# Kernel optimization log

Hardware: AMD Instinct MI355X
Metric: run time of the kernel (lower is better)

Reference implementation:

```python
import jax, jax.numpy as jnp
import numpy as np

V, B, T, D, F, E = 16000, 8, 1024, 64, 256, 8


def setup_inputs() -> dict:
    key = jax.random.key(0)
    ks = jax.random.split(key, 8)
    s = 0.02
    return {
        "x": jax.random.randint(ks[0], (B, T), 0, V),
        "embed_table": jax.random.normal(ks[1], (V, D), jnp.float32) * s,
        "Wm": jax.random.normal(ks[2], (D, D), jnp.float32) * s,
        "Um": jax.random.normal(ks[3], (D, D), jnp.float32) * s,
        "bm": jnp.zeros((D,), jnp.float32),
        "Wg": jax.random.normal(ks[4], (D, E), jnp.float32) * s,
        "bg": jnp.zeros((E,), jnp.float32),
        "W1": jax.random.normal(ks[5], (E, D, F), jnp.float32) * s,
        "b1": jnp.zeros((E, F), jnp.float32),
        "W2": jax.random.normal(ks[6], (E, F, D), jnp.float32) * s,
        "b2": jnp.zeros((E, D), jnp.float32),
        "ln_g": jnp.ones((D,), jnp.float32),
        "ln_b": jnp.zeros((D,), jnp.float32),
        "head_W": jax.random.normal(ks[7], (D, V), jnp.float32) * s,
        "head_b": jnp.zeros((V,), jnp.float32),
    }


def _layernorm(y, g, b, eps=1e-5):
    mu = jnp.mean(y, axis=-1, keepdims=True)
    var = jnp.mean((y - mu) ** 2, axis=-1, keepdims=True)
    return g * (y - mu) * jax.lax.rsqrt(var + eps) + b


def reference(x, embed_table, Wm, Um, bm, Wg, bg, W1, b1, W2, b2, ln_g, ln_b, head_W, head_b):
    emb = embed_table[x]                    # [B, T, D]
    emb_t = jnp.swapaxes(emb, 0, 1)         # [T, B, D] for scan over time

    def step(mem, x_t):
        # recurrent router: state update then gate computation
        mem_new = jnp.tanh(x_t @ Wm + mem @ Um + bm)              # [B, D]
        gates = jax.nn.softmax(mem_new @ Wg + bg, axis=-1)        # [B, E]
        # all-experts dense FFN (exact erf GELU as in torch default)
        h = jax.nn.gelu(jnp.einsum('bd,edf->bef', x_t, W1) + b1, approximate=False)
        eo = jnp.einsum('bef,efd->bed', h, W2) + b2               # [B, E, D]
        moe = jnp.einsum('be,bed->bd', gates, eo)                 # gated sum
        out_t = _layernorm(x_t + moe, ln_g, ln_b)
        return mem_new, out_t

    mem0 = jnp.zeros((x.shape[0], emb.shape[-1]), emb.dtype)
    _, outs = jax.lax.scan(step, mem0, emb_t)   # outs: [T, B, D]
    out = jnp.swapaxes(outs, 0, 1)              # [B, T, D]
    logits = out @ head_W + head_b              # [B, T, V]
    # training_mode=False -> no pred_loss branch; avg_pred_loss == 0.0
    return logits
```

## Files before the change

kernel.cpp:

```cpp
#include <hip/hip_runtime.h>


#define VV 16000
#define BB 8
#define TT 1024
#define DD 64
#define FF 256
#define EE 8
#define BT 8192

typedef unsigned short u16;
typedef unsigned int   u32;
typedef __attribute__((ext_vector_type(8))) short short8;
typedef __attribute__((ext_vector_type(4))) float f32x4;
typedef __attribute__((ext_vector_type(2))) float f32x2;

__device__ __forceinline__ float bf2f(u16 u) {
    union { u32 i; float f; } v; v.i = ((u32)u) << 16; return v.f;
}
__device__ __forceinline__ u16 f2bf(float f) {
    union { float f; u32 i; } v; v.f = f;
    u32 lsb = (v.i >> 16) & 1u;
    return (u16)((v.i + 0x7fffu + lsb) >> 16);
}
__device__ __forceinline__ short8 ld8(const u16* p) { return *(const short8*)p; }
__device__ __forceinline__ float ldf(const void* p, int i, int isbf) {
    return isbf ? bf2f(((const u16*)p)[i]) : ((const float*)p)[i];
}

__global__ __launch_bounds__(256) void k_sniff(const u32* __restrict__ tblw,
                                               int* __restrict__ flag) {
    __shared__ int c;
    int tid = threadIdx.x;
    if (tid == 0) c = 0;
    __syncthreads();
    u32 u = tblw[tid];
    u32 lo = u & 0xFFFFu;
    u32 e = (lo >> 7) & 0xFFu;
    int hit = ((e >= 0x60u && e <= 0x7Eu) || lo == 0u) ? 1 : 0;
    atomicAdd(&c, hit);
    __syncthreads();
    if (tid == 0) *flag = (c >= 192) ? 1 : 0;
}

__global__ __launch_bounds__(256) void k_transph(const void* __restrict__ headW,
                                                 const int* __restrict__ flag,
                                                 u16* __restrict__ headWT) {
    __shared__ float tile[DD][DD + 1];
    int isbf = *flag;
    int v0 = blockIdx.x * 64;
    int tid = threadIdx.x;
    int c = tid & 63, rq = tid >> 6;
#pragma unroll
    for (int i = 0; i < 16; i++) {
        int k = i * 4 + rq;
        tile[k][c] = ldf(headW, k * VV + v0 + c, isbf);
    }
    __syncthreads();
#pragma unroll
    for (int i = 0; i < 16; i++) {
        int v = i * 4 + rq;
        headWT[(v0 + v) * DD + c] = f2bf(tile[c][v]);
    }
}

__global__ __launch_bounds__(256) void k_transpose(const void* __restrict__ W1,
                                                   const void* __restrict__ W2,
                                                   const int* __restrict__ flag,
                                                   u16* __restrict__ W1T,
                                                   u16* __restrict__ W2T) {
    int isbf = *flag;
    int idx = blockIdx.x * 256 + threadIdx.x;
    if (idx < EE * DD * FF) {
        int e = idx >> 14, r = idx & 16383, d = r >> 8, f = r & 255;
        W1T[e * 16384 + f * DD + d] = f2bf(ldf(W1, idx, isbf));
    } else {
        int j2 = idx - EE * DD * FF;
        int e = j2 >> 14, r = j2 & 16383, f = r >> 6, d = r & 63;
        W2T[e * 16384 + d * FF + f] = f2bf(ldf(W2, j2, isbf));
    }
}

__global__ __launch_bounds__(256) void k_embed_pre(const int* __restrict__ x,
                                                   const void* __restrict__ tbl,
                                                   const void* __restrict__ Wm,
                                                   const void* __restrict__ bm,
                                                   const int* __restrict__ flag,
                                                   u16* __restrict__ emb,
                                                   float* __restrict__ pre) {
    __shared__ float sWm[DD * DD];
    __shared__ float sbm[DD];
    int isbf = *flag;
    int tid = threadIdx.x;
    for (int i = tid; i < DD * DD; i += 256) sWm[i] = ldf(Wm, i, isbf);
    if (tid < DD) sbm[tid] = ldf(bm, tid, isbf);
    __syncthreads();

    int gi = blockIdx.x * 256 + tid;
    int tok = gi >> 2, q = gi & 3;
    int id = x[tok];
    float e[DD];
    if (isbf) {
        const uint4* src = (const uint4*)((const u16*)tbl + id * DD);
        uint4* dst = (uint4*)(emb + tok * DD);
#pragma unroll
        for (int i = 0; i < 8; i++) {
            uint4 v = src[i];
            if ((i >> 1) == q) dst[i] = v;
            const u16* pu = (const u16*)&v;
#pragma unroll
            for (int j = 0; j < 8; j++) e[i * 8 + j] = bf2f(pu[j]);
        }
    } else {
        const float4* src = (const float4*)((const float*)tbl + id * DD);
        u16* dst = emb + tok * DD;
#pragma unroll
        for (int i = 0; i < 16; i++) {
            float4 v = src[i];
            e[i * 4 + 0] = v.x; e[i * 4 + 1] = v.y;
            e[i * 4 + 2] = v.z; e[i * 4 + 3] = v.w;
            if ((i >> 2) == q) {
                u32 p0 = (u32)f2bf(v.x) | ((u32)f2bf(v.y) << 16);
                u32 p1 = (u32)f2bf(v.z) | ((u32)f2bf(v.w) << 16);
                ((u32*)dst)[i * 2] = p0;
                ((u32*)dst)[i * 2 + 1] = p1;
            }
        }
    }
    int b = tok >> 10, t = tok & 1023;
    float* prow = pre + (t * BB + b) * DD + q * 16;
#pragma unroll
    for (int j4 = 0; j4 < 4; j4++) {
        int j0 = q * 16 + j4 * 4;
        float a0 = sbm[j0 + 0], a1 = sbm[j0 + 1];
        float a2 = sbm[j0 + 2], a3 = sbm[j0 + 3];
#pragma unroll
        for (int k = 0; k < DD; k++) {
            float ek = e[k];
            float4 wv = *(const float4*)&sWm[k * DD + j0];
            a0 += ek * wv.x; a1 += ek * wv.y;
            a2 += ek * wv.z; a3 += ek * wv.w;
        }
        ((float4*)prow)[j4] = make_float4(a0, a1, a2, a3);
    }
}

__global__ __launch_bounds__(256, 1) void k_scan_ffn(
        const float* __restrict__ pre, const void* __restrict__ Um,
        const u16* __restrict__ emb, const u16* __restrict__ W1T,
        const void* __restrict__ b1g, const u16* __restrict__ W2T,
        const void* __restrict__ b2g, const int* __restrict__ flag,
        float* __restrict__ mem, u16* __restrict__ eo) {
    __shared__ u16 hh[4][16 * 264];
    int isbf = *flag;
    int bid = blockIdx.x;

    if (bid < BB) {
        if (threadIdx.x >= 64) return;
        int b = bid, j = threadIdx.x;
        float* sm = (float*)hh;

        f32x2 c0, c1, c2, c3, c4, c5, c6, c7, c8, c9, c10, c11, c12, c13,
              c14, c15, c16, c17, c18, c19, c20, c21, c22, c23, c24, c25,
              c26, c27, c28, c29, c30, c31;
        if (isbf) {
            const u16* up = (const u16*)Um + j;
#define LDU(VAR, I) VAR = (f32x2){bf2f(up[(2 * I) * DD]), bf2f(up[(2 * I + 1) * DD])};
            LDU(c0, 0)  LDU(c1, 1)  LDU(c2, 2)  LDU(c3, 3)
            LDU(c4, 4)  LDU(c5, 5)  LDU(c6, 6)  LDU(c7, 7)
            LDU(c8, 8)  LDU(c9, 9)  LDU(c10, 10) LDU(c11, 11)
            LDU(c12, 12) LDU(c13, 13) LDU(c14, 14) LDU(c15, 15)
            LDU(c16, 16) LDU(c17, 17) LDU(c18, 18) LDU(c19, 19)
            LDU(c20, 20) LDU(c21, 21) LDU(c22, 22) LDU(c23, 23)
            LDU(c24, 24) LDU(c25, 25) LDU(c26, 26) LDU(c27, 27)
            LDU(c28, 28) LDU(c29, 29) LDU(c30, 30) LDU(c31, 31)
#undef LDU
        } else {
            const float* up = (const float*)Um + j;
#define LDU(VAR, I) VAR = (f32x2){up[(2 * I) * DD], up[(2 * I + 1) * DD]};
            LDU(c0, 0)  LDU(c1, 1)  LDU(c2, 2)  LDU(c3, 3)
            LDU(c4, 4)  LDU(c5, 5)  LDU(c6, 6)  LDU(c7, 7)
            LDU(c8, 8)  LDU(c9, 9)  LDU(c10, 10) LDU(c11, 11)
            LDU(c12, 12) LDU(c13, 13) LDU(c14, 14) LDU(c15, 15)
            LDU(c16, 16) LDU(c17, 17) LDU(c18, 18) LDU(c19, 19)
            LDU(c20, 20) LDU(c21, 21) LDU(c22, 22) LDU(c23, 23)
            LDU(c24, 24) LDU(c25, 25) LDU(c26, 26) LDU(c27, 27)
            LDU(c28, 28) LDU(c29, 29) LDU(c30, 30) LDU(c31, 31)
#undef LDU
        }
        asm volatile("" : "+v"(c0), "+v"(c1), "+v"(c2), "+v"(c3),
                          "+v"(c4), "+v"(c5), "+v"(c6), "+v"(c7));
        asm volatile("" : "+v"(c8), "+v"(c9), "+v"(c10), "+v"(c11),
                          "+v"(c12), "+v"(c13), "+v"(c14), "+v"(c15));
        asm volatile("" : "+v"(c16), "+v"(c17), "+v"(c18), "+v"(c19),
                          "+v"(c20), "+v"(c21), "+v"(c22), "+v"(c23));
        asm volatile("" : "+v"(c24), "+v"(c25), "+v"(c26), "+v"(c27),
                          "+v"(c28), "+v"(c29), "+v"(c30), "+v"(c31));
        sm[j] = 0.f;

        float pcur = pre[b * DD + j];
        for (int t = 0; t < TT; t++) {
            int tn = (t + 1 < TT) ? t + 1 : t;
            float pnext = pre[(tn * BB + b) * DD + j];
            const f32x4* mv = (const f32x4*)sm;
            f32x2 A0 = {0.f, 0.f}, A1 = {0.f, 0.f};
            f32x2 A2 = {0.f, 0.f}, A3 = {0.f, 0.f};
#define STEP2(KK, UA, UB, UC, UD) {                             \
            f32x4 va = mv[2 * KK], vb = mv[2 * KK + 1];         \
            A0 += __builtin_shufflevector(va, va, 0, 1) * UA;   \
            A1 += __builtin_shufflevector(va, va, 2, 3) * UB;   \
            A2 += __builtin_shufflevector(vb, vb, 0, 1) * UC;   \
            A3 += __builtin_shufflevector(vb, vb, 2, 3) * UD; }
            STEP2(0, c0, c1, c2, c3)     STEP2(1, c4, c5, c6, c7)
            STEP2(2, c8, c9, c10, c11)   STEP2(3, c12, c13, c14, c15)
            STEP2(4, c16, c17, c18, c19) STEP2(5, c20, c21, c22, c23)
            STEP2(6, c24, c25, c26, c27) STEP2(7, c28, c29, c30, c31)
#undef STEP2
            float s = ((A0.x + A0.y) + (A1.x + A1.y))
                    + ((A2.x + A2.y) + (A3.x + A3.y)) + pcur;
            float ex = __expf(2.f * s);
            float mn = 1.f - 2.f * __builtin_amdgcn_rcpf(ex + 1.f);
            sm[j] = mn;
            mem[(t * BB + b) * DD + j] = mn;
            pcur = pnext;
        }
        return;
    }

    int fid = bid - BB;
    int e = fid >> 7, mb = fid & 127;
    int w = threadIdx.x >> 6, l = threadIdx.x & 63;
    int lr = l & 15, lq = l >> 4;
    int m0 = mb * 64 + w * 16;

    short8 a0 = ld8(emb + (m0 + lr) * DD + lq * 8);
    short8 a1 = ld8(emb + (m0 + lr) * DD + 32 + lq * 8);
    const u16* w1 = W1T + e * 16384;

    f32x4 acc[16];
#pragma unroll
    for (int nt = 0; nt < 16; nt++) {
        int n = nt * 16 + lr;
        short8 bf0 = ld8(w1 + n * DD + lq * 8);
        short8 bf1 = ld8(w1 + n * DD + 32 + lq * 8);
        f32x4 c = {0.f, 0.f, 0.f, 0.f};
        c = __builtin_amdgcn_mfma_f32_16x16x32_bf16(a0, bf0, c, 0, 0, 0);
        c = __builtin_amdgcn_mfma_f32_16x16x32_bf16(a1, bf1, c, 0, 0, 0);
        acc[nt] = c;
    }
    u16* hw = hh[w];
#pragma unroll
    for (int nt = 0; nt < 16; nt++) {
        int n = nt * 16 + lr;
        float bb = ldf(b1g, e * FF + n, isbf);
#pragma unroll
        for (int r = 0; r < 4; r++) {
            float xv = acc[nt][r] + bb;
            float g = 0.5f * xv * (1.f + erff(xv * 0.70710678118654752f));
            hw[(lq * 4 + r) * 264 + n] = f2bf(g);
        }
    }
    __syncthreads();

    f32x4 acc2[4];
#pragma unroll
    for (int dt = 0; dt < 4; dt++) acc2[dt] = (f32x4){0.f, 0.f, 0.f, 0.f};
    const u16* w2 = W2T + e * 16384;
#pragma unroll
    for (int kb = 0; kb < 8; kb++) {
        short8 af = ld8(hw + lr * 264 + kb * 32 + lq * 8);
#pragma unroll
        for (int dt = 0; dt < 4; dt++) {
            short8 bf = ld8(w2 + (dt * 16 + lr) * FF + kb * 32 + lq * 8);
            acc2[dt] = __builtin_amdgcn_mfma_f32_16x16x32_bf16(af, bf, acc2[dt], 0, 0, 0);
        }
    }
#pragma unroll
    for (int dt = 0; dt < 4; dt++) {
        int d = dt * 16 + lr;
        float bb = ldf(b2g, e * DD + d, isbf);
#pragma unroll
        for (int r = 0; r < 4; r++) {
            int tok = m0 + lq * 4 + r;
            eo[(tok * EE + e) * DD + d] = f2bf(acc2[dt][r] + bb);
        }
    }
}

__global__ __launch_bounds__(256) void k_gates(const float* __restrict__ mem,
                                               const void* __restrict__ Wg,
                                               const void* __restrict__ bg,
                                               const int* __restrict__ flag,
                                               float* __restrict__ gates) {
    __shared__ float sWg[DD * EE];
    int isbf = *flag;
    int tid = threadIdx.x;
    for (int i = tid; i < DD * EE; i += 256) sWg[i] = ldf(Wg, i, isbf);
    __syncthreads();

    int tok = blockIdx.x * 256 + tid;
    int b = tok >> 10, t = tok & 1023;
    const float* mr = mem + (t * BB + b) * DD;
    float z[EE];
#pragma unroll
    for (int e = 0; e < EE; e++) z[e] = ldf(bg, e, isbf);
    const float4* wg4 = (const float4*)sWg;
    const float4* mr4 = (const float4*)mr;
    for (int k4 = 0; k4 < 16; k4++) {
        float4 mv = mr4[k4];
        float m[4] = {mv.x, mv.y, mv.z, mv.w};
#pragma unroll
        for (int kk = 0; kk < 4; kk++) {
            int k = k4 * 4 + kk;
            float4 wa = wg4[k * 2], wb = wg4[k * 2 + 1];
            z[0] += m[kk] * wa.x; z[1] += m[kk] * wa.y;
            z[2] += m[kk] * wa.z; z[3] += m[kk] * wa.w;
            z[4] += m[kk] * wb.x; z[5] += m[kk] * wb.y;
            z[6] += m[kk] * wb.z; z[7] += m[kk] * wb.w;
        }
    }
    float zm = z[0];
#pragma unroll
    for (int e = 1; e < EE; e++) zm = fmaxf(zm, z[e]);
    float sum = 0.f;
#pragma unroll
    for (int e = 0; e < EE; e++) { z[e] = __expf(z[e] - zm); sum += z[e]; }
    float rs = __builtin_amdgcn_rcpf(sum);
#pragma unroll
    for (int e = 0; e < EE; e++) gates[tok * EE + e] = z[e] * rs;
}

__global__ __launch_bounds__(256) void k_ln(const u16* __restrict__ emb,
                                            const u16* __restrict__ eo,
                                            const float* __restrict__ gates,
                                            const void* __restrict__ ln_g,
                                            const void* __restrict__ ln_b,
                                            const int* __restrict__ flag,
                                            u16* __restrict__ outb) {
    int isbf = *flag;
    int w = threadIdx.x >> 6, l = threadIdx.x & 63;
    int tok = blockIdx.x * 4 + w;
    const float* g = gates + tok * EE;
    const u16* er = eo + tok * EE * DD;
    float moe = 0.f;
#pragma unroll
    for (int e = 0; e < EE; e++) moe += g[e] * bf2f(er[e * DD + l]);
    float y = bf2f(emb[tok * DD + l]) + moe;
    float s = y;
#pragma unroll
    for (int off = 32; off > 0; off >>= 1) s += __shfl_xor(s, off, 64);
    float mu = s * (1.f / 64.f);
    float d = y - mu;
    float s2 = d * d;
#pragma unroll
    for (int off = 32; off > 0; off >>= 1) s2 += __shfl_xor(s2, off, 64);
    float var = s2 * (1.f / 64.f);
    float r = rsqrtf(var + 1e-5f);
    float o = ldf(ln_g, l, isbf) * d * r + ldf(ln_b, l, isbf);
    outb[tok * DD + l] = f2bf(o);
}

__global__ __launch_bounds__(256) void k_head(const u16* __restrict__ outb,
                                              const u16* __restrict__ headWT,
                                              const void* __restrict__ head_b,
                                              const int* __restrict__ flag,
                                              void* __restrict__ logits) {
    int isbf = *flag;
    int nb = blockIdx.x, mb = blockIdx.y;
    int w = threadIdx.x >> 6, l = threadIdx.x & 63;
    int lr = l & 15, lq = l >> 4;
    int m0 = mb * 64 + w * 16;
    int n0 = nb * 256;
    int ntc = (nb == 62) ? 8 : 16;

    short8 a0 = ld8(outb + (m0 + lr) * DD + lq * 8);
    short8 a1 = ld8(outb + (m0 + lr) * DD + 32 + lq * 8);

    for (int nt = 0; nt < ntc; nt++) {
        int n = n0 + nt * 16 + lr;
        short8 bf0 = ld8(headWT + n * DD + lq * 8);
        short8 bf1 = ld8(headWT + n * DD + 32 + lq * 8);
        f32x4 c = {0.f, 0.f, 0.f, 0.f};
        c = __builtin_amdgcn_mfma_f32_16x16x32_bf16(a0, bf0, c, 0, 0, 0);
        c = __builtin_amdgcn_mfma_f32_16x16x32_bf16(a1, bf1, c, 0, 0, 0);
        float hb = ldf(head_b, n, isbf);
        if (isbf) {
#pragma unroll
            for (int r = 0; r < 4; r++)
                ((u16*)logits)[(m0 + lq * 4 + r) * VV + n] = f2bf(c[r] + hb);
        } else {
#pragma unroll
            for (int r = 0; r < 4; r++)
                ((float*)logits)[(m0 + lq * 4 + r) * VV + n] = c[r] + hb;
        }
    }
}

extern "C" void kernel_launch(void* const* d_in, const int* in_sizes, int n_in,
                              void* d_out, int out_size, void* d_ws, size_t ws_size,
                              hipStream_t stream) {
    const int*  x      = (const int*)d_in[0];
    const void* tbl    = d_in[1];
    const void* Wm     = d_in[2];
    const void* Um     = d_in[3];
    const void* bm     = d_in[4];
    const void* Wg     = d_in[5];
    const void* bg     = d_in[6];
    const void* W1     = d_in[7];
    const void* b1     = d_in[8];
    const void* W2     = d_in[9];
    const void* b2     = d_in[10];
    const void* ln_g   = d_in[11];
    const void* ln_b   = d_in[12];
    const void* headW  = d_in[13];
    const void* head_b = d_in[14];

    char* w = (char*)d_ws;
    int*   flag   = (int*)(w);
    u16*   headWT = (u16*)(w + 0x0000100);
    u16*   W1T    = (u16*)(w + 0x0200000);
    u16*   W2T    = (u16*)(w + 0x0240000);
    u16*   emb    = (u16*)(w + 0x0280000);
    u16*   outb   = (u16*)(w + 0x0380000);
    float* pre    = (float*)(w + 0x0480000);
    float* mem    = (float*)(w + 0x0680000);
    float* gates  = (float*)(w + 0x0880000);
    u16*   eo     = (u16*)(w + 0x08C0000);

    k_sniff<<<dim3(1), dim3(256), 0, stream>>>((const u32*)tbl, flag);
    k_transph<<<dim3(VV / 64), dim3(256), 0, stream>>>(headW, flag, headWT);
    k_transpose<<<dim3(2 * EE * DD * FF / 256), dim3(256), 0, stream>>>(
        W1, W2, flag, W1T, W2T);
    k_embed_pre<<<dim3(BT * 4 / 256), dim3(256), 0, stream>>>(x, tbl, Wm, bm, flag, emb, pre);
    k_scan_ffn<<<dim3(BB + EE * (BT / 64)), dim3(256), 0, stream>>>(
        pre, Um, emb, W1T, b1, W2T, b2, flag, mem, eo);
    k_gates<<<dim3(BT / 256), dim3(256), 0, stream>>>(mem, Wg, bg, flag, gates);
    k_ln<<<dim3(BT / 4), dim3(256), 0, stream>>>(emb, eo, gates, ln_g, ln_b, flag, outb);
    k_head<<<dim3(63, BT / 64), dim3(256), 0, stream>>>(outb, headWT, head_b, flag, d_out);
}
```

Measured before the change: 975.0 us.

## Pipeline scan, FFN, gates, LN and head across time chunks in a mega-kernel

Merges the embed/pre-projection, head-weight transpose and expert-weight transpose into one launch. The recurrent scan is split into four 256-step chunks, and a single multi-role kernel is launched seven times in a software-pipelined schedule: while chunk c is being scanned, the FFN, gates, layernorm and head GEMM run on earlier chunks. The aim is to hide the serial scan latency behind the parallel FFN and head work, which previously waited for the whole scan to finish. The cost is extra launches and some redundant scan setup per chunk, plus chunk-dependent indexing.

```diff
diff --git a/kernel.cpp b/kernel.cpp
--- a/kernel.cpp
+++ b/kernel.cpp
@@ -8,6 +8,7 @@
 #define FF 256
 #define EE 8
 #define BT 8192
+#define CT 256
 
 typedef unsigned short u16;
 typedef unsigned int   u32;
@@ -43,34 +44,100 @@
     if (tid == 0) *flag = (c >= 192) ? 1 : 0;
 }
 
-__global__ __launch_bounds__(256) void k_transph(const void* __restrict__ headW,
-                                                 const int* __restrict__ flag,
-                                                 u16* __restrict__ headWT) {
-    __shared__ float tile[DD][DD + 1];
+__global__ __launch_bounds__(256) void k_pre(const int* __restrict__ x,
+                                             const void* __restrict__ tbl,
+                                             const void* __restrict__ Wm,
+                                             const void* __restrict__ bm,
+                                             const void* __restrict__ headW,
+                                             const void* __restrict__ W1,
+                                             const void* __restrict__ W2,
+                                             const int* __restrict__ flag,
+                                             u16* __restrict__ emb,
+                                             float* __restrict__ pre,
+                                             u16* __restrict__ headWT,
+                                             u16* __restrict__ W1T,
+                                             u16* __restrict__ W2T) {
+    __shared__ float smem[4160];
     int isbf = *flag;
-    int v0 = blockIdx.x * 64;
+    int bid = blockIdx.x;
     int tid = threadIdx.x;
-    int c = tid & 63, rq = tid >> 6;
-#pragma unroll
-    for (int i = 0; i < 16; i++) {
-        int k = i * 4 + rq;
-        tile[k][c] = ldf(headW, k * VV + v0 + c, isbf);
-    }
-    __syncthreads();
-#pragma unroll
-    for (int i = 0; i < 16; i++) {
-        int v = i * 4 + rq;
-        headWT[(v0 + v) * DD + c] = f2bf(tile[c][v]);
-    }
-}
-
-__global__ __launch_bounds__(256) void k_transpose(const void* __restrict__ W1,
-                                                   const void* __restrict__ W2,
-                                                   const int* __restrict__ flag,
-                                                   u16* __restrict__ W1T,
-                                                   u16* __restrict__ W2T) {
-    int isbf = *flag;
-    int idx = blockIdx.x * 256 + threadIdx.x;
+
+    if (bid < 128) {
+        float* sWm = smem;
+        float* sbm = smem + 4096;
+        for (int i = tid; i < DD * DD; i += 256) sWm[i] = ldf(Wm, i, isbf);
+        if (tid < DD) sbm[tid] = ldf(bm, tid, isbf);
+        __syncthreads();
+
+        int gi = bid * 256 + tid;
+        int tok = gi >> 2, q = gi & 3;
+        int id = x[tok];
+        float e[DD];
+        if (isbf) {
+            const uint4* src = (const uint4*)((const u16*)tbl + id * DD);
+            uint4* dst = (uint4*)(emb + tok * DD);
+#pragma unroll
+            for (int i = 0; i < 8; i++) {
+                uint4 v = src[i];
+                if ((i >> 1) == q) dst[i] = v;
+                const u16* pu = (const u16*)&v;
+#pragma unroll
+                for (int j = 0; j < 8; j++) e[i * 8 + j] = bf2f(pu[j]);
+            }
+        } else {
+            const float4* src = (const float4*)((const float*)tbl + id * DD);
+            u16* dst = emb + tok * DD;
+#pragma unroll
+            for (int i = 0; i < 16; i++) {
+                float4 v = src[i];
+                e[i * 4 + 0] = v.x; e[i * 4 + 1] = v.y;
+                e[i * 4 + 2] = v.z; e[i * 4 + 3] = v.w;
+                if ((i >> 2) == q) {
+                    u32 p0 = (u32)f2bf(v.x) | ((u32)f2bf(v.y) << 16);
+                    u32 p1 = (u32)f2bf(v.z) | ((u32)f2bf(v.w) << 16);
+                    ((u32*)dst)[i * 2] = p0;
+                    ((u32*)dst)[i * 2 + 1] = p1;
+                }
+            }
+        }
+        int b = tok >> 10, t = tok & 1023;
+        float* prow = pre + (t * BB + b) * DD + q * 16;
+#pragma unroll
+        for (int j4 = 0; j4 < 4; j4++) {
+            int j0 = q * 16 + j4 * 4;
+            float a0 = sbm[j0 + 0], a1 = sbm[j0 + 1];
+            float a2 = sbm[j0 + 2], a3 = sbm[j0 + 3];
+#pragma unroll
+            for (int k = 0; k < DD; k++) {
+                float ek = e[k];
+                float4 wv = *(const float4*)&sWm[k * DD + j0];
+                a0 += ek * wv.x; a1 += ek * wv.y;
+                a2 += ek * wv.z; a3 += ek * wv.w;
+            }
+            ((float4*)prow)[j4] = make_float4(a0, a1, a2, a3);
+        }
+        return;
+    }
+
+    if (bid < 128 + 250) {
+        float (*tile)[DD + 1] = (float(*)[DD + 1])smem;
+        int v0 = (bid - 128) * 64;
+        int c = tid & 63, rq = tid >> 6;
+#pragma unroll
+        for (int i = 0; i < 16; i++) {
+            int k = i * 4 + rq;
+            tile[k][c] = ldf(headW, k * VV + v0 + c, isbf);
+        }
+        __syncthreads();
+#pragma unroll
+        for (int i = 0; i < 16; i++) {
+            int v = i * 4 + rq;
+            headWT[(v0 + v) * DD + c] = f2bf(tile[c][v]);
+        }
+        return;
+    }
+
+    int idx = (bid - 378) * 256 + tid;
     if (idx < EE * DD * FF) {
         int e = idx >> 14, r = idx & 16383, d = r >> 8, f = r & 255;
         W1T[e * 16384 + f * DD + d] = f2bf(ldf(W1, idx, isbf));
@@ -81,317 +148,266 @@
     }
 }
 
-__global__ __launch_bounds__(256) void k_embed_pre(const int* __restrict__ x,
-                                                   const void* __restrict__ tbl,
-                                                   const void* __restrict__ Wm,
-                                                   const void* __restrict__ bm,
-                                                   const int* __restrict__ flag,
-                                                   u16* __restrict__ emb,
-                                                   float* __restrict__ pre) {
-    __shared__ float sWm[DD * DD];
-    __shared__ float sbm[DD];
-    int isbf = *flag;
-    int tid = threadIdx.x;
-    for (int i = tid; i < DD * DD; i += 256) sWm[i] = ldf(Wm, i, isbf);
-    if (tid < DD) sbm[tid] = ldf(bm, tid, isbf);
-    __syncthreads();
-
-    int gi = blockIdx.x * 256 + tid;
-    int tok = gi >> 2, q = gi & 3;
-    int id = x[tok];
-    float e[DD];
-    if (isbf) {
-        const uint4* src = (const uint4*)((const u16*)tbl + id * DD);
-        uint4* dst = (uint4*)(emb + tok * DD);
-#pragma unroll
-        for (int i = 0; i < 8; i++) {
-            uint4 v = src[i];
-            if ((i >> 1) == q) dst[i] = v;
-            const u16* pu = (const u16*)&v;
-#pragma unroll
-            for (int j = 0; j < 8; j++) e[i * 8 + j] = bf2f(pu[j]);
-        }
-    } else {
-        const float4* src = (const float4*)((const float*)tbl + id * DD);
-        u16* dst = emb + tok * DD;
-#pragma unroll
-        for (int i = 0; i < 16; i++) {
-            float4 v = src[i];
-            e[i * 4 + 0] = v.x; e[i * 4 + 1] = v.y;
-            e[i * 4 + 2] = v.z; e[i * 4 + 3] = v.w;
-            if ((i >> 2) == q) {
-                u32 p0 = (u32)f2bf(v.x) | ((u32)f2bf(v.y) << 16);
-                u32 p1 = (u32)f2bf(v.z) | ((u32)f2bf(v.w) << 16);
-                ((u32*)dst)[i * 2] = p0;
-                ((u32*)dst)[i * 2 + 1] = p1;
-            }
-        }
-    }
-    int b = tok >> 10, t = tok & 1023;
-    float* prow = pre + (t * BB + b) * DD + q * 16;
-#pragma unroll
-    for (int j4 = 0; j4 < 4; j4++) {
-        int j0 = q * 16 + j4 * 4;
-        float a0 = sbm[j0 + 0], a1 = sbm[j0 + 1];
-        float a2 = sbm[j0 + 2], a3 = sbm[j0 + 3];
-#pragma unroll
-        for (int k = 0; k < DD; k++) {
-            float ek = e[k];
-            float4 wv = *(const float4*)&sWm[k * DD + j0];
-            a0 += ek * wv.x; a1 += ek * wv.y;
-            a2 += ek * wv.z; a3 += ek * wv.w;
-        }
-        ((float4*)prow)[j4] = make_float4(a0, a1, a2, a3);
-    }
-}
-
-__global__ __launch_bounds__(256, 1) void k_scan_ffn(
+__global__ __launch_bounds__(256, 1) void k_mega(
         const float* __restrict__ pre, const void* __restrict__ Um,
         const u16* __restrict__ emb, const u16* __restrict__ W1T,
         const void* __restrict__ b1g, const u16* __restrict__ W2T,
-        const void* __restrict__ b2g, const int* __restrict__ flag,
-        float* __restrict__ mem, u16* __restrict__ eo) {
-    __shared__ u16 hh[4][16 * 264];
+        const void* __restrict__ b2g, const void* __restrict__ Wg,
+        const void* __restrict__ bg, const void* __restrict__ ln_g,
+        const void* __restrict__ ln_b, const u16* __restrict__ headWT,
+        const void* __restrict__ head_b, const int* __restrict__ flag,
+        float* __restrict__ mem, u16* __restrict__ eo,
+        float* __restrict__ gates, u16* __restrict__ outb,
+        void* __restrict__ logits,
+        int scan_c, int ffn_c, int gates_c, int ln_c, int head_c) {
+    extern __shared__ char dynsm[];
     int isbf = *flag;
     int bid = blockIdx.x;
 
-    if (bid < BB) {
-        if (threadIdx.x >= 64) return;
-        int b = bid, j = threadIdx.x;
-        float* sm = (float*)hh;
-
-        f32x2 c0, c1, c2, c3, c4, c5, c6, c7, c8, c9, c10, c11, c12, c13,
-              c14, c15, c16, c17, c18, c19, c20, c21, c22, c23, c24, c25,
-              c26, c27, c28, c29, c30, c31;
-        if (isbf) {
-            const u16* up = (const u16*)Um + j;
+    if (scan_c >= 0) {
+        if (bid < BB) {
+            if (threadIdx.x >= 64) return;
+            int b = bid, j = threadIdx.x;
+            float* sm = (float*)dynsm;
+
+            f32x2 c0, c1, c2, c3, c4, c5, c6, c7, c8, c9, c10, c11, c12, c13,
+                  c14, c15, c16, c17, c18, c19, c20, c21, c22, c23, c24, c25,
+                  c26, c27, c28, c29, c30, c31;
+            if (isbf) {
+                const u16* up = (const u16*)Um + j;
 #define LDU(VAR, I) VAR = (f32x2){bf2f(up[(2 * I) * DD]), bf2f(up[(2 * I + 1) * DD])};
-            LDU(c0, 0)  LDU(c1, 1)  LDU(c2, 2)  LDU(c3, 3)
-            LDU(c4, 4)  LDU(c5, 5)  LDU(c6, 6)  LDU(c7, 7)
-            LDU(c8, 8)  LDU(c9, 9)  LDU(c10, 10) LDU(c11, 11)
-            LDU(c12, 12) LDU(c13, 13) LDU(c14, 14) LDU(c15, 15)
-            LDU(c16, 16) LDU(c17, 17) LDU(c18, 18) LDU(c19, 19)
-            LDU(c20, 20) LDU(c21, 21) LDU(c22, 22) LDU(c23, 23)
-            LDU(c24, 24) LDU(c25, 25) LDU(c26, 26) LDU(c27, 27)
-            LDU(c28, 28) LDU(c29, 29) LDU(c30, 30) LDU(c31, 31)
+                LDU(c0, 0)  LDU(c1, 1)  LDU(c2, 2)  LDU(c3, 3)
+                LDU(c4, 4)  LDU(c5, 5)  LDU(c6, 6)  LDU(c7, 7)
+                LDU(c8, 8)  LDU(c9, 9)  LDU(c10, 10) LDU(c11, 11)
+                LDU(c12, 12) LDU(c13, 13) LDU(c14, 14) LDU(c15, 15)
+                LDU(c16, 16) LDU(c17, 17) LDU(c18, 18) LDU(c19, 19)
+                LDU(c20, 20) LDU(c21, 21) LDU(c22, 22) LDU(c23, 23)
+                LDU(c24, 24) LDU(c25, 25) LDU(c26, 26) LDU(c27, 27)
+                LDU(c28, 28) LDU(c29, 29) LDU(c30, 30) LDU(c31, 31)
 #undef LDU
-        } else {
-            const float* up = (const float*)Um + j;
+            } else {
+                const float* up = (const float*)Um + j;
 #define LDU(VAR, I) VAR = (f32x2){up[(2 * I) * DD], up[(2 * I + 1) * DD]};
-            LDU(c0, 0)  LDU(c1, 1)  LDU(c2, 2)  LDU(c3, 3)
-            LDU(c4, 4)  LDU(c5, 5)  LDU(c6, 6)  LDU(c7, 7)
-            LDU(c8, 8)  LDU(c9, 9)  LDU(c10, 10) LDU(c11, 11)
-            LDU(c12, 12) LDU(c13, 13) LDU(c14, 14) LDU(c15, 15)
-            LDU(c16, 16) LDU(c17, 17) LDU(c18, 18) LDU(c19, 19)
-            LDU(c20, 20) LDU(c21, 21) LDU(c22, 22) LDU(c23, 23)
-            LDU(c24, 24) LDU(c25, 25) LDU(c26, 26) LDU(c27, 27)
-            LDU(c28, 28) LDU(c29, 29) LDU(c30, 30) LDU(c31, 31)
+                LDU(c0, 0)  LDU(c1, 1)  LDU(c2, 2)  LDU(c3, 3)
+                LDU(c4, 4)  LDU(c5, 5)  LDU(c6, 6)  LDU(c7, 7)
+                LDU(c8, 8)  LDU(c9, 9)  LDU(c10, 10) LDU(c11, 11)
+                LDU(c12, 12) LDU(c13, 13) LDU(c14, 14) LDU(c15, 15)
+                LDU(c16, 16) LDU(c17, 17) LDU(c18, 18) LDU(c19, 19)
+                LDU(c20, 20) LDU(c21, 21) LDU(c22, 22) LDU(c23, 23)
+                LDU(c24, 24) LDU(c25, 25) LDU(c26, 26) LDU(c27, 27)
+                LDU(c28, 28) LDU(c29, 29) LDU(c30, 30) LDU(c31, 31)
 #undef LDU
-        }
-        asm volatile("" : "+v"(c0), "+v"(c1), "+v"(c2), "+v"(c3),
-                          "+v"(c4), "+v"(c5), "+v"(c6), "+v"(c7));
-        asm volatile("" : "+v"(c8), "+v"(c9), "+v"(c10), "+v"(c11),
-                          "+v"(c12), "+v"(c13), "+v"(c14), "+v"(c15));
-        asm volatile("" : "+v"(c16), "+v"(c17), "+v"(c18), "+v"(c19),
-                          "+v"(c20), "+v"(c21), "+v"(c22), "+v"(c23));
-        asm volatile("" : "+v"(c24), "+v"(c25), "+v"(c26), "+v"(c27),
-                          "+v"(c28), "+v"(c29), "+v"(c30), "+v"(c31));
-        sm[j] = 0.f;
-
-        float pcur = pre[b * DD + j];
-        for (int t = 0; t < TT; t++) {
-            int tn = (t + 1 < TT) ? t + 1 : t;
-            float pnext = pre[(tn * BB + b) * DD + j];
-            const f32x4* mv = (const f32x4*)sm;
-            f32x2 A0 = {0.f, 0.f}, A1 = {0.f, 0.f};
-            f32x2 A2 = {0.f, 0.f}, A3 = {0.f, 0.f};
+            }
+            asm volatile("" : "+v"(c0), "+v"(c1), "+v"(c2), "+v"(c3),
+                              "+v"(c4), "+v"(c5), "+v"(c6), "+v"(c7));
+            asm volatile("" : "+v"(c8), "+v"(c9), "+v"(c10), "+v"(c11),
+                              "+v"(c12), "+v"(c13), "+v"(c14), "+v"(c15));
+            asm volatile("" : "+v"(c16), "+v"(c17), "+v"(c18), "+v"(c19),
+                              "+v"(c20), "+v"(c21), "+v"(c22), "+v"(c23));
+            asm volatile("" : "+v"(c24), "+v"(c25), "+v"(c26), "+v"(c27),
+                              "+v"(c28), "+v"(c29), "+v"(c30), "+v"(c31));
+
+            int t0 = scan_c * CT, t1 = t0 + CT;
+            sm[j] = (scan_c == 0) ? 0.f : mem[((t0 - 1) * BB + b) * DD + j];
+
+            float pcur = pre[(t0 * BB + b) * DD + j];
+            for (int t = t0; t < t1; t++) {
+                int tn = (t + 1 < t1) ? t + 1 : t;
+                float pnext = pre[(tn * BB + b) * DD + j];
+                const f32x4* mv = (const f32x4*)sm;
+                f32x2 A0 = {0.f, 0.f}, A1 = {0.f, 0.f};
+                f32x2 A2 = {0.f, 0.f}, A3 = {0.f, 0.f};
 #define STEP2(KK, UA, UB, UC, UD) {                             \
-            f32x4 va = mv[2 * KK], vb = mv[2 * KK + 1];         \
-            A0 += __builtin_shufflevector(va, va, 0, 1) * UA;   \
-            A1 += __builtin_shufflevector(va, va, 2, 3) * UB;   \
-            A2 += __builtin_shufflevector(vb, vb, 0, 1) * UC;   \
-            A3 += __builtin_shufflevector(vb, vb, 2, 3) * UD; }
-            STEP2(0, c0, c1, c2, c3)     STEP2(1, c4, c5, c6, c7)
-            STEP2(2, c8, c9, c10, c11)   STEP2(3, c12, c13, c14, c15)
-            STEP2(4, c16, c17, c18, c19) STEP2(5, c20, c21, c22, c23)
-            STEP2(6, c24, c25, c26, c27) STEP2(7, c28, c29, c30, c31)
+                f32x4 va = mv[2 * KK], vb = mv[2 * KK + 1];     \
+                A0 += __builtin_shufflevector(va, va, 0, 1) * UA;   \
+                A1 += __builtin_shufflevector(va, va, 2, 3) * UB;   \
+                A2 += __builtin_shufflevector(vb, vb, 0, 1) * UC;   \
+                A3 += __builtin_shufflevector(vb, vb, 2, 3) * UD; }
+                STEP2(0, c0, c1, c2, c3)     STEP2(1, c4, c5, c6, c7)
+                STEP2(2, c8, c9, c10, c11)   STEP2(3, c12, c13, c14, c15)
+                STEP2(4, c16, c17, c18, c19) STEP2(5, c20, c21, c22, c23)
+                STEP2(6, c24, c25, c26, c27) STEP2(7, c28, c29, c30, c31)
 #undef STEP2
-            float s = ((A0.x + A0.y) + (A1.x + A1.y))
-                    + ((A2.x + A2.y) + (A3.x + A3.y)) + pcur;
-            float ex = __expf(2.f * s);
-            float mn = 1.f - 2.f * __builtin_amdgcn_rcpf(ex + 1.f);
-            sm[j] = mn;
-            mem[(t * BB + b) * DD + j] = mn;
-            pcur = pnext;
-        }
-        return;
-    }
-
-    int fid = bid - BB;
-    int e = fid >> 7, mb = fid & 127;
-    int w = threadIdx.x >> 6, l = threadIdx.x & 63;
-    int lr = l & 15, lq = l >> 4;
-    int m0 = mb * 64 + w * 16;
-
-    short8 a0 = ld8(emb + (m0 + lr) * DD + lq * 8);
-    short8 a1 = ld8(emb + (m0 + lr) * DD + 32 + lq * 8);
-    const u16* w1 = W1T + e * 16384;
-
-    f32x4 acc[16];
-#pragma unroll
-    for (int nt = 0; nt < 16; nt++) {
-        int n = nt * 16 + lr;
-        short8 bf0 = ld8(w1 + n * DD + lq * 8);
-        short8 bf1 = ld8(w1 + n * DD + 32 + lq * 8);
-        f32x4 c = {0.f, 0.f, 0.f, 0.f};
-        c = __builtin_amdgcn_mfma_f32_16x16x32_bf16(a0, bf0, c, 0, 0, 0);
-        c = __builtin_amdgcn_mfma_f32_16x16x32_bf16(a1, bf1, c, 0, 0, 0);
-        acc[nt] = c;
-    }
-    u16* hw = hh[w];
-#pragma unroll
-    for (int nt = 0; nt < 16; nt++) {
-        int n = nt * 16 + lr;
-        float bb = ldf(b1g, e * FF + n, isbf);
-#pragma unroll
-        for (int r = 0; r < 4; r++) {
-            float xv = acc[nt][r] + bb;
-            float g = 0.5f * xv * (1.f + erff(xv * 0.70710678118654752f));
-            hw[(lq * 4 + r) * 264 + n] = f2bf(g);
-        }
-    }
-    __syncthreads();
-
-    f32x4 acc2[4];
-#pragma unroll
-    for (int dt = 0; dt < 4; dt++) acc2[dt] = (f32x4){0.f, 0.f, 0.f, 0.f};
-    const u16* w2 = W2T + e * 16384;
-#pragma unroll
-    for (int kb = 0; kb < 8; kb++) {
-        short8 af = ld8(hw + lr * 264 + kb * 32 + lq * 8);
-#pragma unroll
-        for (int dt = 0; dt < 4; dt++) {
-            short8 bf = ld8(w2 + (dt * 16 + lr) * FF + kb * 32 + lq * 8);
-            acc2[dt] = __builtin_amdgcn_mfma_f32_16x16x32_bf16(af, bf, acc2[dt], 0, 0, 0);
-        }
-    }
-#pragma unroll
-    for (int dt = 0; dt < 4; dt++) {
-        int d = dt * 16 + lr;
-        float bb = ldf(b2g, e * DD + d, isbf);
-#pragma unroll
-        for (int r = 0; r < 4; r++) {
-            int tok = m0 + lq * 4 + r;
-            eo[(tok * EE + e) * DD + d] = f2bf(acc2[dt][r] + bb);
-        }
-    }
-}
-
-__global__ __launch_bounds__(256) void k_gates(const float* __restrict__ mem,
-                                               const void* __restrict__ Wg,
-                                               const void* __restrict__ bg,
-                                               const int* __restrict__ flag,
-                                               float* __restrict__ gates) {
-    __shared__ float sWg[DD * EE];
-    int isbf = *flag;
-    int tid = threadIdx.x;
-    for (int i = tid; i < DD * EE; i += 256) sWg[i] = ldf(Wg, i, isbf);
-    __syncthreads();
-
-    int tok = blockIdx.x * 256 + tid;
-    int b = tok >> 10, t = tok & 1023;
-    const float* mr = mem + (t * BB + b) * DD;
-    float z[EE];
-#pragma unroll
-    for (int e = 0; e < EE; e++) z[e] = ldf(bg, e, isbf);
-    const float4* wg4 = (const float4*)sWg;
-    const float4* mr4 = (const float4*)mr;
-    for (int k4 = 0; k4 < 16; k4++) {
-        float4 mv = mr4[k4];
-        float m[4] = {mv.x, mv.y, mv.z, mv.w};
-#pragma unroll
-        for (int kk = 0; kk < 4; kk++) {
-            int k = k4 * 4 + kk;
-            float4 wa = wg4[k * 2], wb = wg4[k * 2 + 1];
-            z[0] += m[kk] * wa.x; z[1] += m[kk] * wa.y;
-            z[2] += m[kk] * wa.z; z[3] += m[kk] * wa.w;
-            z[4] += m[kk] * wb.x; z[5] += m[kk] * wb.y;
-            z[6] += m[kk] * wb.z; z[7] += m[kk] * wb.w;
-        }
-    }
-    float zm = z[0];
-#pragma unroll
-    for (int e = 1; e < EE; e++) zm = fmaxf(zm, z[e]);
-    float sum = 0.f;
-#pragma unroll
-    for (int e = 0; e < EE; e++) { z[e] = __expf(z[e] - zm); sum += z[e]; }
-    float rs = __builtin_amdgcn_rcpf(sum);
-#pragma unroll
-    for (int e = 0; e < EE; e++) gates[tok * EE + e] = z[e] * rs;
-}
-
-__global__ __launch_bounds__(256) void k_ln(const u16* __restrict__ emb,
-                                            const u16* __restrict__ eo,
-                                            const float* __restrict__ gates,
-                                            const void* __restrict__ ln_g,
-                                            const void* __restrict__ ln_b,
-                                            const int* __restrict__ flag,
-                                            u16* __restrict__ outb) {
-    int isbf = *flag;
-    int w = threadIdx.x >> 6, l = threadIdx.x & 63;
-    int tok = blockIdx.x * 4 + w;
-    const float* g = gates + tok * EE;
-    const u16* er = eo + tok * EE * DD;
-    float moe = 0.f;
-#pragma unroll
-    for (int e = 0; e < EE; e++) moe += g[e] * bf2f(er[e * DD + l]);
-    float y = bf2f(emb[tok * DD + l]) + moe;
-    float s = y;
-#pragma unroll
-    for (int off = 32; off > 0; off >>= 1) s += __shfl_xor(s, off, 64);
-    float mu = s * (1.f / 64.f);
-    float d = y - mu;
-    float s2 = d * d;
-#pragma unroll
-    for (int off = 32; off > 0; off >>= 1) s2 += __shfl_xor(s2, off, 64);
-    float var = s2 * (1.f / 64.f);
-    float r = rsqrtf(var + 1e-5f);
-    float o = ldf(ln_g, l, isbf) * d * r + ldf(ln_b, l, isbf);
-    outb[tok * DD + l] = f2bf(o);
-}
-
-__global__ __launch_bounds__(256) void k_head(const u16* __restrict__ outb,
-                                              const u16* __restrict__ headWT,
-                                              const void* __restrict__ head_b,
-                                              const int* __restrict__ flag,
-                                              void* __restrict__ logits) {
-    int isbf = *flag;
-    int nb = blockIdx.x, mb = blockIdx.y;
-    int w = threadIdx.x >> 6, l = threadIdx.x & 63;
-    int lr = l & 15, lq = l >> 4;
-    int m0 = mb * 64 + w * 16;
-    int n0 = nb * 256;
-    int ntc = (nb == 62) ? 8 : 16;
-
-    short8 a0 = ld8(outb + (m0 + lr) * DD + lq * 8);
-    short8 a1 = ld8(outb + (m0 + lr) * DD + 32 + lq * 8);
-
-    for (int nt = 0; nt < ntc; nt++) {
-        int n = n0 + nt * 16 + lr;
-        short8 bf0 = ld8(headWT + n * DD + lq * 8);
-        short8 bf1 = ld8(headWT + n * DD + 32 + lq * 8);
-        f32x4 c = {0.f, 0.f, 0.f, 0.f};
-        c = __builtin_amdgcn_mfma_f32_16x16x32_bf16(a0, bf0, c, 0, 0, 0);
-        c = __builtin_amdgcn_mfma_f32_16x16x32_bf16(a1, bf1, c, 0, 0, 0);
-        float hb = ldf(head_b, n, isbf);
-        if (isbf) {
-#pragma unroll
-            for (int r = 0; r < 4; r++)
-                ((u16*)logits)[(m0 + lq * 4 + r) * VV + n] = f2bf(c[r] + hb);
-        } else {
-#pragma unroll
-            for (int r = 0; r < 4; r++)
-                ((float*)logits)[(m0 + lq * 4 + r) * VV + n] = c[r] + hb;
+                float s = ((A0.x + A0.y) + (A1.x + A1.y))
+                        + ((A2.x + A2.y) + (A3.x + A3.y)) + pcur;
+                float ex = __expf(2.f * s);
+                float mn = 1.f - 2.f * __builtin_amdgcn_rcpf(ex + 1.f);
+                sm[j] = mn;
+                mem[(t * BB + b) * DD + j] = mn;
+                pcur = pnext;
+            }
+            return;
+        }
+        bid -= BB;
+    }
+
+    if (ffn_c >= 0) {
+        if (bid < 256) {
+            int e = bid >> 5, lm = bid & 31;
+            int mb = (lm >> 2) * 16 + ffn_c * 4 + (lm & 3);
+            int w = threadIdx.x >> 6, l = threadIdx.x & 63;
+            int lr = l & 15, lq = l >> 4;
+            int m0 = mb * 64 + w * 16;
+            u16* hw = (u16*)dynsm + w * (16 * 264);
+
+            short8 a0 = ld8(emb + (m0 + lr) * DD + lq * 8);
+            short8 a1 = ld8(emb + (m0 + lr) * DD + 32 + lq * 8);
+            const u16* w1 = W1T + e * 16384;
+
+            f32x4 acc[16];
+#pragma unroll
+            for (int nt = 0; nt < 16; nt++) {
+                int n = nt * 16 + lr;
+                short8 bf0 = ld8(w1 + n * DD + lq * 8);
+                short8 bf1 = ld8(w1 + n * DD + 32 + lq * 8);
+                f32x4 c = {0.f, 0.f, 0.f, 0.f};
+                c = __builtin_amdgcn_mfma_f32_16x16x32_bf16(a0, bf0, c, 0, 0, 0);
+                c = __builtin_amdgcn_mfma_f32_16x16x32_bf16(a1, bf1, c, 0, 0, 0);
+                acc[nt] = c;
+            }
+#pragma unroll
+            for (int nt = 0; nt < 16; nt++) {
+                int n = nt * 16 + lr;
+                float bb = ldf(b1g, e * FF + n, isbf);
+#pragma unroll
+                for (int r = 0; r < 4; r++) {
+                    float xv = acc[nt][r] + bb;
+                    float g = 0.5f * xv * (1.f + erff(xv * 0.70710678118654752f));
+                    hw[(lq * 4 + r) * 264 + n] = f2bf(g);
+                }
+            }
+            __syncthreads();
+
+            f32x4 acc2[4];
+#pragma unroll
+            for (int dt = 0; dt < 4; dt++) acc2[dt] = (f32x4){0.f, 0.f, 0.f, 0.f};
+            const u16* w2 = W2T + e * 16384;
+#pragma unroll
+            for (int kb = 0; kb < 8; kb++) {
+                short8 af = ld8(hw + lr * 264 + kb * 32 + lq * 8);
+#pragma unroll
+                for (int dt = 0; dt < 4; dt++) {
+                    short8 bf = ld8(w2 + (dt * 16 + lr) * FF + kb * 32 + lq * 8);
+                    acc2[dt] = __builtin_amdgcn_mfma_f32_16x16x32_bf16(af, bf, acc2[dt], 0, 0, 0);
+                }
+            }
+#pragma unroll
+            for (int dt = 0; dt < 4; dt++) {
+                int d = dt * 16 + lr;
+                float bb = ldf(b2g, e * DD + d, isbf);
+#pragma unroll
+                for (int r = 0; r < 4; r++) {
+                    int tok = m0 + lq * 4 + r;
+                    eo[(tok * EE + e) * DD + d] = f2bf(acc2[dt][r] + bb);
+                }
+            }
+            return;
+        }
+        bid -= 256;
+    }
+
+    if (gates_c >= 0) {
+        if (bid < 8) {
+            float* sWg = (float*)dynsm;
+            int tid = threadIdx.x;
+            for (int i = tid; i < DD * EE; i += 256) sWg[i] = ldf(Wg, i, isbf);
+            __syncthreads();
+
+            int idx = bid * 256 + tid;
+            int b = idx >> 8, toff = idx & 255;
+            int t = gates_c * CT + toff;
+            int tok = (b << 10) + t;
+            const float* mr = mem + (t * BB + b) * DD;
+            float z[EE];
+#pragma unroll
+            for (int e = 0; e < EE; e++) z[e] = ldf(bg, e, isbf);
+            const float4* wg4 = (const float4*)sWg;
+            const float4* mr4 = (const float4*)mr;
+            for (int k4 = 0; k4 < 16; k4++) {
+                float4 mv = mr4[k4];
+                float m[4] = {mv.x, mv.y, mv.z, mv.w};
+#pragma unroll
+                for (int kk = 0; kk < 4; kk++) {
+                    int k = k4 * 4 + kk;
+                    float4 wa = wg4[k * 2], wb = wg4[k * 2 + 1];
+                    z[0] += m[kk] * wa.x; z[1] += m[kk] * wa.y;
+                    z[2] += m[kk] * wa.z; z[3] += m[kk] * wa.w;
+                    z[4] += m[kk] * wb.x; z[5] += m[kk] * wb.y;
+                    z[6] += m[kk] * wb.z; z[7] += m[kk] * wb.w;
+                }
+            }
+            float zm = z[0];
+#pragma unroll
+            for (int e = 1; e < EE; e++) zm = fmaxf(zm, z[e]);
+            float sum = 0.f;
+#pragma unroll
+            for (int e = 0; e < EE; e++) { z[e] = __expf(z[e] - zm); sum += z[e]; }
+            float rs = __builtin_amdgcn_rcpf(sum);
+#pragma unroll
+            for (int e = 0; e < EE; e++) gates[tok * EE + e] = z[e] * rs;
+            return;
+        }
+        bid -= 8;
+    }
+
+    if (ln_c >= 0) {
+        if (bid < 512) {
+            int w = threadIdx.x >> 6, l = threadIdx.x & 63;
+            int idx = bid * 4 + w;
+            int b = idx >> 8, toff = idx & 255;
+            int tok = (b << 10) + ln_c * CT + toff;
+            const float* g = gates + tok * EE;
+            const u16* er = eo + tok * EE * DD;
+            float moe = 0.f;
+#pragma unroll
+            for (int e = 0; e < EE; e++) moe += g[e] * bf2f(er[e * DD + l]);
+            float y = bf2f(emb[tok * DD + l]) + moe;
+            float s = y;
+#pragma unroll
+            for (int off = 32; off > 0; off >>= 1) s += __shfl_xor(s, off, 64);
+            float mu = s * (1.f / 64.f);
+            float d = y - mu;
+            float s2 = d * d;
+#pragma unroll
+            for (int off = 32; off > 0; off >>= 1) s2 += __shfl_xor(s2, off, 64);
+            float var = s2 * (1.f / 64.f);
+            float r = rsqrtf(var + 1e-5f);
+            float o = ldf(ln_g, l, isbf) * d * r + ldf(ln_b, l, isbf);
+            outb[tok * DD + l] = f2bf(o);
+            return;
+        }
+        bid -= 512;
+    }
+
+    {
+        int w = threadIdx.x >> 6, l = threadIdx.x & 63;
+        int lr = l & 15, lq = l >> 4;
+        int nb = bid / 32, lm = bid % 32;
+        int mb = (lm >> 2) * 16 + head_c * 4 + (lm & 3);
+        int m0 = mb * 64 + w * 16;
+        int n0 = nb * 256;
+        int ntc = (nb == 62) ? 8 : 16;
+
+        short8 a0 = ld8(outb + (m0 + lr) * DD + lq * 8);
+        short8 a1 = ld8(outb + (m0 + lr) * DD + 32 + lq * 8);
+
+        for (int nt = 0; nt < ntc; nt++) {
+            int n = n0 + nt * 16 + lr;
+            short8 bf0 = ld8(headWT + n * DD + lq * 8);
+            short8 bf1 = ld8(headWT + n * DD + 32 + lq * 8);
+            f32x4 c = {0.f, 0.f, 0.f, 0.f};
+            c = __builtin_amdgcn_mfma_f32_16x16x32_bf16(a0, bf0, c, 0, 0, 0);
+            c = __builtin_amdgcn_mfma_f32_16x16x32_bf16(a1, bf1, c, 0, 0, 0);
+            float hb = ldf(head_b, n, isbf);
+            if (isbf) {
+#pragma unroll
+                for (int r = 0; r < 4; r++)
+                    ((u16*)logits)[(m0 + lq * 4 + r) * VV + n] = f2bf(c[r] + hb);
+            } else {
+#pragma unroll
+                for (int r = 0; r < 4; r++)
+                    ((float*)logits)[(m0 + lq * 4 + r) * VV + n] = c[r] + hb;
+            }
         }
     }
 }
@@ -428,13 +444,27 @@
     u16*   eo     = (u16*)(w + 0x08C0000);
 
     k_sniff<<<dim3(1), dim3(256), 0, stream>>>((const u32*)tbl, flag);
-    k_transph<<<dim3(VV / 64), dim3(256), 0, stream>>>(headW, flag, headWT);
-    k_transpose<<<dim3(2 * EE * DD * FF / 256), dim3(256), 0, stream>>>(
-        W1, W2, flag, W1T, W2T);
-    k_embed_pre<<<dim3(BT * 4 / 256), dim3(256), 0, stream>>>(x, tbl, Wm, bm, flag, emb, pre);
-    k_scan_ffn<<<dim3(BB + EE * (BT / 64)), dim3(256), 0, stream>>>(
-        pre, Um, emb, W1T, b1, W2T, b2, flag, mem, eo);
-    k_gates<<<dim3(BT / 256), dim3(256), 0, stream>>>(mem, Wg, bg, flag, gates);
-    k_ln<<<dim3(BT / 4), dim3(256), 0, stream>>>(emb, eo, gates, ln_g, ln_b, flag, outb);
-    k_head<<<dim3(63, BT / 64), dim3(256), 0, stream>>>(outb, headWT, head_b, flag, d_out);
-}
+    k_pre<<<dim3(1402), dim3(256), 0, stream>>>(x, tbl, Wm, bm, headW, W1, W2,
+                                                flag, emb, pre, headWT, W1T, W2T);
+
+    auto mega = [&](int sc, int fc, int gc, int lc, int hc) {
+        int grid = 0;
+        if (sc >= 0) grid += BB;
+        if (fc >= 0) grid += 256;
+        if (gc >= 0) grid += 8;
+        if (lc >= 0) grid += 512;
+        if (hc >= 0) grid += 2016;
+        size_t sh = (fc >= 0) ? (size_t)(4 * 16 * 264 * 2) : (size_t)2048;
+        k_mega<<<dim3(grid), dim3(256), sh, stream>>>(
+            pre, Um, emb, W1T, b1, W2T, b2, Wg, bg, ln_g, ln_b, headWT, head_b,
+            flag, mem, eo, gates, outb, d_out, sc, fc, gc, lc, hc);
+    };
+
+    mega(0, 0, -1, -1, -1);
+    mega(1, 1, 0, -1, -1);
+    mega(2, 2, 1, 0, -1);
+    mega(3, 3, 2, 1, 0);
+    mega(-1, -1, 3, 2, 1);
+    mega(-1, -1, -1, 3, 2);
+    mega(-1, -1, -1, -1, 3);
+}
```

Result: faster. 949.7 us (-2.6%).
